# Performance work log

Hardware: AMD Instinct MI355X
Metric: run time of the kernel (lower is better)

Reference implementation:

```python
import jax, jax.numpy as jnp
import numpy as np

K = 5          # window_size
PAD = K // 2

def _unfold(t):
    # torch.nn.functional.unfold(t, K, stride=1, padding=PAD)
    # t: [B,C,H,W] -> [B, C*K*K, H*W], patch index flattened channel-major (c, ki, kj)
    B, C, H, W = t.shape
    tp = jnp.pad(t, ((0, 0), (0, 0), (PAD, PAD), (PAD, PAD)))
    cols = jnp.stack([tp[:, :, i:i + H, j:j + W] for i in range(K) for j in range(K)], axis=2)  # [B,C,K*K,H,W]
    return cols.reshape(B, C * K * K, H * W)

def _fold(cols, H, W):
    # torch.nn.functional.fold(cols, (H,W), K, padding=PAD): overlap-add inverse of unfold
    B, CKK, _ = cols.shape
    C = CKK // (K * K)
    c = cols.reshape(B, C, K, K, H, W)
    outp = jnp.zeros((B, C, H + 2 * PAD, W + 2 * PAD), dtype=cols.dtype)
    for i in range(K):
        for j in range(K):
            outp = outp.at[:, :, i:i + H, j:j + W].add(c[:, :, i, j])
    return outp[:, :, PAD:PAD + H, PAD:PAD + W]

def setup_inputs() -> dict:
    key = jax.random.key(0)
    ks = jax.random.split(key, 8)
    C = 64
    x = jax.random.normal(ks[0], (4, 128, 128, C), dtype=jnp.float32)
    Wq = jax.random.normal(ks[1], (C // 8, C), dtype=jnp.float32) * 0.1
    bq = jax.random.normal(ks[2], (C // 8,), dtype=jnp.float32) * 0.1
    Wk = jax.random.normal(ks[3], (C // 8, C), dtype=jnp.float32) * 0.1
    bk = jax.random.normal(ks[4], (C // 8,), dtype=jnp.float32) * 0.1
    Wv = jax.random.normal(ks[5], (C, C), dtype=jnp.float32) * 0.1
    bv = jax.random.normal(ks[6], (C,), dtype=jnp.float32) * 0.1
    gamma = jax.random.normal(ks[7], (1,), dtype=jnp.float32)
    return {"x": x, "Wq": Wq, "bq": bq, "Wk": Wk, "bk": bk, "Wv": Wv, "bv": bv, "gamma": gamma}

def reference(x, Wq, bq, Wk, bk, Wv, bv, gamma):
    # channels_last input -> NCHW
    xc = jnp.transpose(x, (0, 3, 1, 2))
    B, C, H, W = xc.shape
    pdim = K * K
    # 1x1 convs == per-pixel linear
    q = jnp.einsum('bchw,oc->bohw', xc, Wq) + bq[None, :, None, None]
    k = jnp.einsum('bchw,oc->bohw', xc, Wk) + bk[None, :, None, None]
    v = jnp.einsum('bchw,oc->bohw', xc, Wv) + bv[None, :, None, None]
    # unfold then the module's raw (patch_dim, C) reinterpretation reshape
    qp = _unfold(q).transpose(0, 2, 1).reshape(B, H, W, pdim, -1)
    kp = _unfold(k).transpose(0, 2, 1).reshape(B, H, W, pdim, -1)
    vp = _unfold(v).transpose(0, 2, 1).reshape(B, H, W, pdim, -1)
    logits = jnp.einsum('bhwnc,bhwmc->bhwnm', qp, kp)
    attn = jax.nn.softmax(logits, axis=-1)
    local = jnp.einsum('bhwnm,bhwmc->bhwnc', attn, vp)  # [B,H,W,25,C]
    cols = local.reshape(B, H * W, -1).transpose(0, 2, 1)  # raw reinterpretation back to fold layout
    folded = _fold(cols, H, W)
    out = gamma[0] * folded + xc
    out = jnp.transpose(out, (0, 2, 3, 1))  # back to channels_last
    return out, attn
```

## Files before the change

### kernel.cpp

```cpp
#include <hip/hip_runtime.h>
#include <hip/hip_fp16.h>

#define NPIX (4*128*128)
#define OUT_ELEMS (NPIX*64)

typedef _Float16 half8 __attribute__((ext_vector_type(8)));
typedef float f32x16 __attribute__((ext_vector_type(16)));

__device__ __forceinline__ int div25(int v) { return (v * 5243) >> 17; }
__device__ __forceinline__ int div5(int v)  { return (v * 205) >> 10; }

__global__ __launch_bounds__(256) void k1_qkv(
    const float* __restrict__ x,
    const float* __restrict__ Wq, const float* __restrict__ bq,
    const float* __restrict__ Wk, const float* __restrict__ bk,
    const float* __restrict__ Wv, const float* __restrict__ bv,
    float* __restrict__ qws, float* __restrict__ kws, float* __restrict__ vws,
    float* __restrict__ out_init)
{
    __shared__ float sWv[64 * 65];
    __shared__ float sWqk[16 * 65];

    int t = threadIdx.x;
    for (int e = t; e < 64 * 64; e += 256) sWv[(e >> 6) * 65 + (e & 63)] = Wv[e];
    for (int e = t; e < 8 * 64; e += 256) {
        int o = e >> 6, c = e & 63;
        sWqk[o * 65 + c]       = Wq[e];
        sWqk[(o + 8) * 65 + c] = Wk[e];
    }
    __syncthreads();

    int wid = t >> 6, lane = t & 63;
    bool isq = lane < 8;
    bool isk = (lane >= 8) && (lane < 16);
    const float* wr  = sWv + lane * 65;
    const float* wr2 = sWqk + (lane & 7) * 65 + (isk ? 8 * 65 : 0);
    float bvl = bv[lane];
    float bql = isq ? bq[lane] : (isk ? bk[lane - 8] : 0.f);

    #pragma unroll 1
    for (int i = 0; i < 8; ++i) {
        int pix = blockIdx.x * 32 + wid * 8 + i;
        float xv = x[(size_t)pix * 64 + lane];
        float accv = bvl, accq = bql;
        #pragma unroll
        for (int cc = 0; cc < 64; ++cc) {
            float xc = __shfl(xv, cc);
            accv = fmaf(xc, wr[cc], accv);
            accq = fmaf(xc, wr2[cc], accq);
        }
        vws[(size_t)pix * 64 + lane] = accv;
        if (out_init) out_init[(size_t)pix * 64 + lane] = xv;
        if (isq)      qws[(size_t)pix * 8 + lane] = accq;
        else if (isk) kws[(size_t)pix * 8 + (lane - 8)] = accq;
    }
}

__global__ __launch_bounds__(256) void k2_attn_ws(
    const float* __restrict__ qws, const float* __restrict__ kws,
    const float* __restrict__ vws,
    float* __restrict__ attn, __half* __restrict__ lws)
{
    __shared__ float smem[4 * 1984];

    int tid = threadIdx.x, wid = tid >> 6, lane = tid & 63;
    float* W   = smem + wid * 1984;
    float* Qs  = W;
    float* Kt  = W + 200;
    float* E   = W + 424;
    float* R   = W + 1152;
    __half* Vth = (__half*)(W + 1184);
    __half* LBh = Vth;

    int pix = blockIdx.x * 4 + wid;
    int b = pix >> 14, y = (pix >> 7) & 127, x = pix & 127;
    size_t ibase = (size_t)b << 14;

    if (lane < 25) {
        float* er = E + lane * 28;
        er[25] = 0.f; er[26] = 0.f; er[27] = 0.f;
    }
    if (lane < 28) E[700 + lane] = 0.f;

    const float* vb = vws + ibase * 64;
    int vbase = lane * 25;
    #pragma unroll
    for (int p = 0; p < 25; ++p) {
        int i5 = div5(p);
        int yy = y + i5 - 2, xx = x + (p - i5 * 5) - 2;
        float val = 0.f;
        if ((unsigned)yy < 128u && (unsigned)xx < 128u)
            val = vb[(size_t)(((yy << 7) + xx) * 64 + lane)];
        Vth[vbase + p] = __float2half(val);
    }

    const float* qb = qws + ibase * 8;
    const float* kb = kws + ibase * 8;
    #pragma unroll
    for (int i = 0; i < 4; ++i) {
        int e = lane + (i << 6);
        if (e < 200) {
            int cq = div25(e), p = e - cq * 25;
            int i5 = div5(p);
            int yy = y + i5 - 2, xx = x + (p - i5 * 5) - 2;
            float qv = 0.f, kv = 0.f;
            if ((unsigned)yy < 128u && (unsigned)xx < 128u) {
                int off = ((yy << 7) + xx) * 8 + cq;
                qv = qb[off];
                kv = kb[off];
            }
            Qs[e] = qv;
            Kt[(e & 7) * 28 + (e >> 3)] = kv;
        }
    }

    {
        bool act = lane < 50;
        int m_l = (lane < 25) ? lane : lane - 25;
        int n0  = (lane < 25) ? 0 : 13;
        float kreg[8];
        #pragma unroll
        for (int cc = 0; cc < 8; ++cc)
            kreg[cc] = Kt[cc * 28 + m_l];
        #pragma unroll
        for (int t = 0; t < 13; ++t) {
            int n = n0 + t;
            bool ok = act && (n < 25);
            int nn = ok ? n : 0;
            const float4* qr = (const float4*)(Qs + (nn << 3));
            float4 q0 = qr[0], q1 = qr[1];
            float s = q0.x * kreg[0] + q0.y * kreg[1] + q0.z * kreg[2] + q0.w * kreg[3]
                    + q1.x * kreg[4] + q1.y * kreg[5] + q1.z * kreg[6] + q1.w * kreg[7];
            if (ok) E[n * 28 + m_l] = s;
        }
    }

    if (lane < 50) {
        int n = lane >> 1, hf = lane & 1;
        float* row = E + n * 28;
        int m0 = hf * 12;
        float mx = -3.4e38f;
        #pragma unroll
        for (int t = 0; t < 13; ++t) mx = fmaxf(mx, row[m0 + t]);
        mx = fmaxf(mx, __shfl_xor(mx, 1));
        float sum = 0.f;
        #pragma unroll
        for (int t = 0; t < 13; ++t) {
            int m = m0 + t;
            float ev = __expf(row[m] - mx);
            row[m] = ev;
            sum += (hf && t == 0) ? 0.f : ev;
        }
        sum += __shfl_xor(sum, 1);
        R[n] = 1.f / sum;
    }

    float* ab = attn + (size_t)pix * 625;
    #pragma unroll
    for (int i = 0; i < 10; ++i) {
        int e = lane + (i << 6);
        if (e < 625) {
            int n = div25(e), m = e - n * 25;
            ab[e] = E[n * 28 + m] * R[n];
        }
    }

    int h  = lane >> 5;
    int lo = lane & 31;

    half8 afr[2];
    #pragma unroll
    for (int s = 0; s < 2; ++s) {
        const float4* ep = (const float4*)(E + lo * 28 + 16 * s + 8 * h);
        float4 p0 = ep[0], p1 = ep[1];
        afr[s][0] = (_Float16)p0.x; afr[s][1] = (_Float16)p0.y;
        afr[s][2] = (_Float16)p0.z; afr[s][3] = (_Float16)p0.w;
        afr[s][4] = (_Float16)p1.x; afr[s][5] = (_Float16)p1.y;
        afr[s][6] = (_Float16)p1.z; afr[s][7] = (_Float16)p1.w;
    }

    f32x16 acc0 = {0,0,0,0,0,0,0,0,0,0,0,0,0,0,0,0};
    f32x16 acc1 = {0,0,0,0,0,0,0,0,0,0,0,0,0,0,0,0};
    #pragma unroll
    for (int s = 0; s < 2; ++s) {
        half8 b0, b1;
        #pragma unroll
        for (int j = 0; j < 8; ++j) {
            int k = 16 * s + 8 * h + j;
            bool ok = (k < 25);
            int off = ok ? (((16 * s + j) << 6) + (h << 9)) : 0;
            _Float16 v0 = Vth[off + lo];
            _Float16 v1 = Vth[off + 32 + lo];
            b0[j] = ok ? v0 : (_Float16)0.f;
            b1[j] = ok ? v1 : (_Float16)0.f;
        }
        acc0 = __builtin_amdgcn_mfma_f32_32x32x16_f16(afr[s], b0, acc0, 0, 0, 0);
        acc1 = __builtin_amdgcn_mfma_f32_32x32x16_f16(afr[s], b1, acc1, 0, 0, 0);
    }

    #pragma unroll
    for (int r16 = 0; r16 < 16; ++r16) {
        int row = (r16 & 3) + 8 * (r16 >> 2) + 4 * h;
        if (row < 25) {
            float rn = R[row];
            LBh[(row << 6) + lo]      = __float2half(acc0[r16] * rn);
            LBh[(row << 6) + 32 + lo] = __float2half(acc1[r16] * rn);
        }
    }

    #pragma unroll
    for (int p = 0; p < 25; ++p)
        lws[((size_t)p * NPIX + (size_t)pix) * 64 + lane] = LBh[lane * 25 + p];
}

__global__ __launch_bounds__(256) void k3_fold(
    const float* __restrict__ x, const __half* __restrict__ lws,
    const float* __restrict__ gamma, float* __restrict__ out)
{
    int tid = threadIdx.x, wid = tid >> 6, lane = tid & 63;
    int pix4 = (blockIdx.x * 4 + wid) * 4;
    int b = pix4 >> 14, y = (pix4 >> 7) & 127, x0 = pix4 & 127;
    int sub = lane >> 4;
    int ch4 = (lane & 15) << 2;
    size_t ibase = (size_t)b << 14;

    float s0 = 0.f, s1 = 0.f, s2 = 0.f, s3 = 0.f;
    #pragma unroll
    for (int i = 0; i < 5; ++i) {
        int cy = y + 2 - i;
        if ((unsigned)cy >= 128u) continue;
        #pragma unroll
        for (int j = 0; j < 5; ++j) {
            int cx = x0 + sub + 2 - j;
            if ((unsigned)cx < 128u) {
                size_t src = ((size_t)(i * 5 + j) * NPIX + (ibase + (size_t)((cy << 7) + cx))) * 64 + ch4;
                float2 w = *(const float2*)(lws + src);
                __half2 h0 = *(__half2*)&w.x, h1 = *(__half2*)&w.y;
                float2 fa = __half22float2(h0), fb = __half22float2(h1);
                s0 += fa.x; s1 += fa.y; s2 += fb.x; s3 += fb.y;
            }
        }
    }

    float g = gamma[0];
    size_t o = ((size_t)pix4 + sub) * 64 + ch4;
    float4 xv = *(const float4*)(x + o);
    float4 r;
    r.x = fmaf(g, s0, xv.x);
    r.y = fmaf(g, s1, xv.y);
    r.z = fmaf(g, s2, xv.z);
    r.w = fmaf(g, s3, xv.w);
    *(float4*)(out + o) = r;
}

__device__ __forceinline__ void attn_core_fb(
    int lane, int y, int x, size_t ibase,
    const float* __restrict__ qws, const float* __restrict__ kws,
    const float* __restrict__ vws, float* __restrict__ attn,
    float* V, float* Qs, float* Ks, float* E, float* R, float vr[25])
{
    const float* vb = vws + ibase * 64;
    #pragma unroll
    for (int p = 0; p < 25; ++p) {
        int i5 = div5(p);
        int yy = y + i5 - 2, xx = x + (p - i5 * 5) - 2;
        float val = 0.f;
        if ((unsigned)yy < 128u && (unsigned)xx < 128u)
            val = vb[(size_t)(((yy << 7) + xx) * 64 + lane)];
        V[p * 65 + lane] = val;
    }
    const float* qb = qws + ibase * 8;
    const float* kb = kws + ibase * 8;
    #pragma unroll
    for (int i = 0; i < 4; ++i) {
        int e = lane + (i << 6);
        if (e < 200) {
            int cq = div25(e), p = e - cq * 25;
            int i5 = div5(p);
            int yy = y + i5 - 2, xx = x + (p - i5 * 5) - 2;
            float qv = 0.f, kv = 0.f;
            if ((unsigned)yy < 128u && (unsigned)xx < 128u) {
                int off = ((yy << 7) + xx) * 8 + cq;
                qv = qb[off];
                kv = kb[off];
            }
            Qs[e] = qv;
            Ks[e] = kv;
        }
    }
    #pragma unroll
    for (int m = 0; m < 25; ++m) {
        int g = (m << 6) + lane;
        int cv = div25(g), p = g - cv * 25;
        vr[m] = V[p * 65 + cv];
    }
    #pragma unroll
    for (int i = 0; i < 10; ++i) {
        int e = lane + (i << 6);
        if (e < 625) {
            int n = div25(e), m = e - n * 25;
            const float4* qr = (const float4*)(Qs + (n << 3));
            const float4* kr = (const float4*)(Ks + (m << 3));
            float4 q0 = qr[0], q1 = qr[1], k0 = kr[0], k1 = kr[1];
            E[n * 28 + m] = q0.x * k0.x + q0.y * k0.y + q0.z * k0.z + q0.w * k0.w
                          + q1.x * k1.x + q1.y * k1.y + q1.z * k1.z + q1.w * k1.w;
        }
    }
    if (lane < 25) {
        float* row = E + lane * 28;
        float mx = -3.4e38f;
        #pragma unroll
        for (int m = 0; m < 25; ++m) mx = fmaxf(mx, row[m]);
        float s = 0.f;
        #pragma unroll
        for (int m = 0; m < 25; ++m) {
            float ev = __expf(row[m] - mx);
            row[m] = ev;
            s += ev;
        }
        R[lane] = 1.f / s;
    }
    float* ab = attn + (ibase + (size_t)((y << 7) + x)) * 625;
    #pragma unroll
    for (int i = 0; i < 10; ++i) {
        int e = lane + (i << 6);
        if (e < 625) {
            int n = div25(e), m = e - n * 25;
            ab[e] = E[n * 28 + m] * R[n];
        }
    }
}

__global__ __launch_bounds__(256) void k2_attn_atomic(
    const float* __restrict__ qws, const float* __restrict__ kws,
    const float* __restrict__ vws, const float* __restrict__ gamma,
    float* __restrict__ out, float* __restrict__ attn)
{
    __shared__ float sV[4][1632];
    __shared__ float sQ[4][200];
    __shared__ float sK[4][200];
    __shared__ float sE[4][704];
    __shared__ float sR[4][32];

    int tid = threadIdx.x, wid = tid >> 6, lane = tid & 63;
    int pix = blockIdx.x * 4 + wid;
    int b = pix >> 14, y = (pix >> 7) & 127, x = pix & 127;
    size_t ibase = (size_t)b << 14;

    float vr[25];
    attn_core_fb(lane, y, x, ibase, qws, kws, vws, attn,
                 sV[wid], sQ[wid], sK[wid], sE[wid], sR[wid], vr);

    float g0 = gamma[0];
    float acc[25];
    float* E = sE[wid];
    float* R = sR[wid];
    #pragma unroll
    for (int n = 0; n < 25; ++n) {
        const float4* er = (const float4*)(E + n * 28);
        float aa = E[n * 28 + 24] * vr[24];
        #pragma unroll
        for (int q4 = 0; q4 < 6; ++q4) {
            float4 ev = er[q4];
            aa = fmaf(ev.x, vr[q4 * 4 + 0], aa);
            aa = fmaf(ev.y, vr[q4 * 4 + 1], aa);
            aa = fmaf(ev.z, vr[q4 * 4 + 2], aa);
            aa = fmaf(ev.w, vr[q4 * 4 + 3], aa);
        }
        acc[n] = aa * (R[n] * g0);
    }

    float* LB = sV[wid];
    #pragma unroll
    for (int n = 0; n < 25; ++n) LB[(n << 6) + lane] = acc[n];

    float* ob = out + ibase * 64;
    #pragma unroll
    for (int p = 0; p < 25; ++p) {
        int i5 = div5(p);
        int ty = y + i5 - 2, tx = x + (p - i5 * 5) - 2;
        if ((unsigned)ty < 128u && (unsigned)tx < 128u)
            atomicAdd(ob + (size_t)(((ty << 7) + tx) * 64 + lane), LB[lane * 25 + p]);
    }
}

extern "C" void kernel_launch(void* const* d_in, const int* in_sizes, int n_in,
                              void* d_out, int out_size, void* d_ws, size_t ws_size,
                              hipStream_t stream)
{
    const float* x  = (const float*)d_in[0];
    const float* Wq = (const float*)d_in[1];
    const float* bq = (const float*)d_in[2];
    const float* Wk = (const float*)d_in[3];
    const float* bk = (const float*)d_in[4];
    const float* Wv = (const float*)d_in[5];
    const float* bv = (const float*)d_in[6];
    const float* gm = (const float*)d_in[7];

    float* out  = (float*)d_out;
    float* attn = out + OUT_ELEMS;

    float* qws = (float*)d_ws;
    float* kws = qws + (size_t)NPIX * 8;
    float* vws = kws + (size_t)NPIX * 8;
    __half* lws = (__half*)(vws + (size_t)NPIX * 64);

    const size_t need = (size_t)NPIX * 80 * 4 + (size_t)NPIX * 1600 * 2;

    if (ws_size >= need) {
        hipLaunchKernelGGL(k1_qkv, dim3(NPIX / 32), dim3(256), 0, stream,
                           x, Wq, bq, Wk, bk, Wv, bv, qws, kws, vws, (float*)nullptr);
        hipLaunchKernelGGL(k2_attn_ws, dim3(NPIX / 4), dim3(256), 0, stream,
                           qws, kws, vws, attn, lws);
        hipLaunchKernelGGL(k3_fold, dim3(NPIX / 16), dim3(256), 0, stream,
                           x, lws, gm, out);
    } else {
        hipLaunchKernelGGL(k1_qkv, dim3(NPIX / 32), dim3(256), 0, stream,
                           x, Wq, bq, Wk, bk, Wv, bv, qws, kws, vws, out);
        hipLaunchKernelGGL(k2_attn_atomic, dim3(NPIX / 4), dim3(256), 0, stream,
                           qws, kws, vws, gm, out, attn);
    }
}
```

Before: 279.1 us.

## Fuse fold into MFMA attention kernel via atomic adds, drop fp16 workspace

Removes the separate fold kernel and the large half-precision per-patch workspace. The MFMA attention kernel now scales its output by gamma and scatters it into the output with float atomic adds. k1 initializes the output with x. This avoids writing and re-reading a 25x-expanded intermediate, at the cost of contended global atomics (each output element gets up to 25 adds) and a nondeterministic summation order.

Result: slower. 485.1 us (+73.8%).

```diff
diff --git a/kernel.cpp b/kernel.cpp
--- a/kernel.cpp
+++ b/kernel.cpp
@@ -50,16 +50,16 @@
             accq = fmaf(xc, wr2[cc], accq);
         }
         vws[(size_t)pix * 64 + lane] = accv;
-        if (out_init) out_init[(size_t)pix * 64 + lane] = xv;
+        out_init[(size_t)pix * 64 + lane] = xv;
         if (isq)      qws[(size_t)pix * 8 + lane] = accq;
         else if (isk) kws[(size_t)pix * 8 + (lane - 8)] = accq;
     }
 }
 
-__global__ __launch_bounds__(256) void k2_attn_ws(
+__global__ __launch_bounds__(256) void k2_attn_fold(
     const float* __restrict__ qws, const float* __restrict__ kws,
-    const float* __restrict__ vws,
-    float* __restrict__ attn, __half* __restrict__ lws)
+    const float* __restrict__ vws, const float* __restrict__ gamma,
+    float* __restrict__ attn, float* __restrict__ out)
 {
     __shared__ float smem[4 * 1984];
 
@@ -198,181 +198,16 @@
         acc1 = __builtin_amdgcn_mfma_f32_32x32x16_f16(afr[s], b1, acc1, 0, 0, 0);
     }
 
+    float g0 = gamma[0];
     #pragma unroll
     for (int r16 = 0; r16 < 16; ++r16) {
         int row = (r16 & 3) + 8 * (r16 >> 2) + 4 * h;
         if (row < 25) {
-            float rn = R[row];
-            LBh[(row << 6) + lo]      = __float2half(acc0[r16] * rn);
-            LBh[(row << 6) + 32 + lo] = __float2half(acc1[r16] * rn);
-        }
-    }
-
-    #pragma unroll
-    for (int p = 0; p < 25; ++p)
-        lws[((size_t)p * NPIX + (size_t)pix) * 64 + lane] = LBh[lane * 25 + p];
-}
-
-__global__ __launch_bounds__(256) void k3_fold(
-    const float* __restrict__ x, const __half* __restrict__ lws,
-    const float* __restrict__ gamma, float* __restrict__ out)
-{
-    int tid = threadIdx.x, wid = tid >> 6, lane = tid & 63;
-    int pix4 = (blockIdx.x * 4 + wid) * 4;
-    int b = pix4 >> 14, y = (pix4 >> 7) & 127, x0 = pix4 & 127;
-    int sub = lane >> 4;
-    int ch4 = (lane & 15) << 2;
-    size_t ibase = (size_t)b << 14;
-
-    float s0 = 0.f, s1 = 0.f, s2 = 0.f, s3 = 0.f;
-    #pragma unroll
-    for (int i = 0; i < 5; ++i) {
-        int cy = y + 2 - i;
-        if ((unsigned)cy >= 128u) continue;
-        #pragma unroll
-        for (int j = 0; j < 5; ++j) {
-            int cx = x0 + sub + 2 - j;
-            if ((unsigned)cx < 128u) {
-                size_t src = ((size_t)(i * 5 + j) * NPIX + (ibase + (size_t)((cy << 7) + cx))) * 64 + ch4;
-                float2 w = *(const float2*)(lws + src);
-                __half2 h0 = *(__half2*)&w.x, h1 = *(__half2*)&w.y;
-                float2 fa = __half22float2(h0), fb = __half22float2(h1);
-                s0 += fa.x; s1 += fa.y; s2 += fb.x; s3 += fb.y;
-            }
-        }
-    }
-
-    float g = gamma[0];
-    size_t o = ((size_t)pix4 + sub) * 64 + ch4;
-    float4 xv = *(const float4*)(x + o);
-    float4 r;
-    r.x = fmaf(g, s0, xv.x);
-    r.y = fmaf(g, s1, xv.y);
-    r.z = fmaf(g, s2, xv.z);
-    r.w = fmaf(g, s3, xv.w);
-    *(float4*)(out + o) = r;
-}
-
-__device__ __forceinline__ void attn_core_fb(
-    int lane, int y, int x, size_t ibase,
-    const float* __restrict__ qws, const float* __restrict__ kws,
-    const float* __restrict__ vws, float* __restrict__ attn,
-    float* V, float* Qs, float* Ks, float* E, float* R, float vr[25])
-{
-    const float* vb = vws + ibase * 64;
-    #pragma unroll
-    for (int p = 0; p < 25; ++p) {
-        int i5 = div5(p);
-        int yy = y + i5 - 2, xx = x + (p - i5 * 5) - 2;
-        float val = 0.f;
-        if ((unsigned)yy < 128u && (unsigned)xx < 128u)
-            val = vb[(size_t)(((yy << 7) + xx) * 64 + lane)];
-        V[p * 65 + lane] = val;
-    }
-    const float* qb = qws + ibase * 8;
-    const float* kb = kws + ibase * 8;
-    #pragma unroll
-    for (int i = 0; i < 4; ++i) {
-        int e = lane + (i << 6);
-        if (e < 200) {
-            int cq = div25(e), p = e - cq * 25;
-            int i5 = div5(p);
-            int yy = y + i5 - 2, xx = x + (p - i5 * 5) - 2;
-            float qv = 0.f, kv = 0.f;
-            if ((unsigned)yy < 128u && (unsigned)xx < 128u) {
-                int off = ((yy << 7) + xx) * 8 + cq;
-                qv = qb[off];
-                kv = kb[off];
-            }
-            Qs[e] = qv;
-            Ks[e] = kv;
-        }
-    }
-    #pragma unroll
-    for (int m = 0; m < 25; ++m) {
-        int g = (m << 6) + lane;
-        int cv = div25(g), p = g - cv * 25;
-        vr[m] = V[p * 65 + cv];
-    }
-    #pragma unroll
-    for (int i = 0; i < 10; ++i) {
-        int e = lane + (i << 6);
-        if (e < 625) {
-            int n = div25(e), m = e - n * 25;
-            const float4* qr = (const float4*)(Qs + (n << 3));
-            const float4* kr = (const float4*)(Ks + (m << 3));
-            float4 q0 = qr[0], q1 = qr[1], k0 = kr[0], k1 = kr[1];
-            E[n * 28 + m] = q0.x * k0.x + q0.y * k0.y + q0.z * k0.z + q0.w * k0.w
-                          + q1.x * k1.x + q1.y * k1.y + q1.z * k1.z + q1.w * k1.w;
-        }
-    }
-    if (lane < 25) {
-        float* row = E + lane * 28;
-        float mx = -3.4e38f;
-        #pragma unroll
-        for (int m = 0; m < 25; ++m) mx = fmaxf(mx, row[m]);
-        float s = 0.f;
-        #pragma unroll
-        for (int m = 0; m < 25; ++m) {
-            float ev = __expf(row[m] - mx);
-            row[m] = ev;
-            s += ev;
-        }
-        R[lane] = 1.f / s;
-    }
-    float* ab = attn + (ibase + (size_t)((y << 7) + x)) * 625;
-    #pragma unroll
-    for (int i = 0; i < 10; ++i) {
-        int e = lane + (i << 6);
-        if (e < 625) {
-            int n = div25(e), m = e - n * 25;
-            ab[e] = E[n * 28 + m] * R[n];
-        }
-    }
-}
-
-__global__ __launch_bounds__(256) void k2_attn_atomic(
-    const float* __restrict__ qws, const float* __restrict__ kws,
-    const float* __restrict__ vws, const float* __restrict__ gamma,
-    float* __restrict__ out, float* __restrict__ attn)
-{
-    __shared__ float sV[4][1632];
-    __shared__ float sQ[4][200];
-    __shared__ float sK[4][200];
-    __shared__ float sE[4][704];
-    __shared__ float sR[4][32];
-
-    int tid = threadIdx.x, wid = tid >> 6, lane = tid & 63;
-    int pix = blockIdx.x * 4 + wid;
-    int b = pix >> 14, y = (pix >> 7) & 127, x = pix & 127;
-    size_t ibase = (size_t)b << 14;
-
-    float vr[25];
-    attn_core_fb(lane, y, x, ibase, qws, kws, vws, attn,
-                 sV[wid], sQ[wid], sK[wid], sE[wid], sR[wid], vr);
-
-    float g0 = gamma[0];
-    float acc[25];
-    float* E = sE[wid];
-    float* R = sR[wid];
-    #pragma unroll
-    for (int n = 0; n < 25; ++n) {
-        const float4* er = (const float4*)(E + n * 28);
-        float aa = E[n * 28 + 24] * vr[24];
-        #pragma unroll
-        for (int q4 = 0; q4 < 6; ++q4) {
-            float4 ev = er[q4];
-            aa = fmaf(ev.x, vr[q4 * 4 + 0], aa);
-            aa = fmaf(ev.y, vr[q4 * 4 + 1], aa);
-            aa = fmaf(ev.z, vr[q4 * 4 + 2], aa);
-            aa = fmaf(ev.w, vr[q4 * 4 + 3], aa);
-        }
-        acc[n] = aa * (R[n] * g0);
-    }
-
-    float* LB = sV[wid];
-    #pragma unroll
-    for (int n = 0; n < 25; ++n) LB[(n << 6) + lane] = acc[n];
+            float rg = R[row] * g0;
+            LBh[(row << 6) + lo]      = __float2half(acc0[r16] * rg);
+            LBh[(row << 6) + 32 + lo] = __float2half(acc1[r16] * rg);
+        }
+    }
 
     float* ob = out + ibase * 64;
     #pragma unroll
@@ -380,7 +215,8 @@
         int i5 = div5(p);
         int ty = y + i5 - 2, tx = x + (p - i5 * 5) - 2;
         if ((unsigned)ty < 128u && (unsigned)tx < 128u)
-            atomicAdd(ob + (size_t)(((ty << 7) + tx) * 64 + lane), LB[lane * 25 + p]);
+            atomicAdd(ob + (size_t)(((ty << 7) + tx) * 64 + lane),
+                      __half2float(LBh[lane * 25 + p]));
     }
 }
 
@@ -403,21 +239,9 @@
     float* qws = (float*)d_ws;
     float* kws = qws + (size_t)NPIX * 8;
     float* vws = kws + (size_t)NPIX * 8;
-    __half* lws = (__half*)(vws + (size_t)NPIX * 64);
-
-    const size_t need = (size_t)NPIX * 80 * 4 + (size_t)NPIX * 1600 * 2;
-
-    if (ws_size >= need) {
-        hipLaunchKernelGGL(k1_qkv, dim3(NPIX / 32), dim3(256), 0, stream,
-                           x, Wq, bq, Wk, bk, Wv, bv, qws, kws, vws, (float*)nullptr);
-        hipLaunchKernelGGL(k2_attn_ws, dim3(NPIX / 4), dim3(256), 0, stream,
-                           qws, kws, vws, attn, lws);
-        hipLaunchKernelGGL(k3_fold, dim3(NPIX / 16), dim3(256), 0, stream,
-                           x, lws, gm, out);
-    } else {
-        hipLaunchKernelGGL(k1_qkv, dim3(NPIX / 32), dim3(256), 0, stream,
-                           x, Wq, bq, Wk, bk, Wv, bv, qws, kws, vws, out);
-        hipLaunchKernelGGL(k2_attn_atomic, dim3(NPIX / 4), dim3(256), 0, stream,
-                           qws, kws, vws, gm, out, attn);
-    }
+
+    hipLaunchKernelGGL(k1_qkv, dim3(NPIX / 32), dim3(256), 0, stream,
+                       x, Wq, bq, Wk, bk, Wv, bv, qws, kws, vws, out);
+    hipLaunchKernelGGL(k2_attn_fold, dim3(NPIX / 4), dim3(256), 0, stream,
+                       qws, kws, vws, gm, attn, out);
 }
```
